# Kernel tuning notes

Measured on AMD Instinct MI355X. Metric: run time of the kernel, lower is better.

The kernel has to match this reference:

```python
import jax, jax.numpy as jnp
import numpy as np

B, T, F_IN = 256, 168, 128
H = 512            # encoder hidden per direction; decoder hidden = 2H
OUT = 1
L_OUT = 48
SCALE = 0.05


def _lstm_scan(x, Wih, Whh, b, h0, c0):
    # x: [T, B, F]; PyTorch LSTM gate order i, f, g, o
    def step(carry, xt):
        h, c = carry
        g = xt @ Wih.T + h @ Whh.T + b
        i, f, gg, o = jnp.split(g, 4, axis=-1)
        c = jax.nn.sigmoid(f) * c + jax.nn.sigmoid(i) * jnp.tanh(gg)
        h = jax.nn.sigmoid(o) * jnp.tanh(c)
        return (h, c), h
    (hT, cT), ys = jax.lax.scan(step, (h0, c0), x)
    return ys, hT, cT


def setup_inputs() -> dict:
    key = jax.random.key(0)
    ks = jax.random.split(key, 16)
    r = lambda k, shp: (jax.random.normal(k, shp, dtype=jnp.float32) * SCALE)
    return {
        "input_seq": jax.random.normal(ks[0], (B, T, F_IN), dtype=jnp.float32),
        "enc_Wih_f": r(ks[1], (4 * H, F_IN)),
        "enc_Whh_f": r(ks[2], (4 * H, H)),
        "enc_bih_f": r(ks[3], (4 * H,)),
        "enc_bhh_f": r(ks[4], (4 * H,)),
        "enc_Wih_b": r(ks[5], (4 * H, F_IN)),
        "enc_Whh_b": r(ks[6], (4 * H, H)),
        "enc_bih_b": r(ks[7], (4 * H,)),
        "enc_bhh_b": r(ks[8], (4 * H,)),
        "dec_Wih": r(ks[9], (4 * 2 * H, OUT)),
        "dec_Whh": r(ks[10], (4 * 2 * H, 2 * H)),
        "dec_bih": r(ks[11], (4 * 2 * H,)),
        "dec_bhh": r(ks[12], (4 * 2 * H,)),
        "fc_W": r(ks[13], (OUT, 2 * H)),
        "fc_b": r(ks[14], (OUT,)),
        "output_length": L_OUT,
    }


def reference(input_seq, enc_Wih_f, enc_Whh_f, enc_bih_f, enc_bhh_f,
              enc_Wih_b, enc_Whh_b, enc_bih_b, enc_bhh_b,
              dec_Wih, dec_Whh, dec_bih, dec_bhh, fc_W, fc_b, output_length):
    b = input_seq.shape[0]
    h = enc_Whh_f.shape[1]
    x = jnp.transpose(input_seq, (1, 0, 2))  # [T, B, F]
    h0 = jnp.zeros((b, h), input_seq.dtype)
    c0 = jnp.zeros((b, h), input_seq.dtype)
    # bidirectional encoder (final hidden/cell only are used downstream)
    _, hf, cf = _lstm_scan(x, enc_Wih_f, enc_Whh_f, enc_bih_f + enc_bhh_f, h0, c0)
    _, hb, cb = _lstm_scan(x[::-1], enc_Wih_b, enc_Whh_b, enc_bih_b + enc_bhh_b, h0, c0)
    # _cat_hidden: concat fwd/bwd states along feature dim -> decoder init state [B, 2H]
    hd = jnp.concatenate([hf, hb], axis=-1)
    cd = jnp.concatenate([cf, cb], axis=-1)
    bd = dec_bih + dec_bhh
    x0 = jnp.zeros((b, fc_W.shape[0]), input_seq.dtype)  # initial decoder input = zeros

    def dec_step(carry, _):
        hh, cc, xt = carry
        g = xt @ dec_Wih.T + hh @ dec_Whh.T + bd
        i, f, gg, o = jnp.split(g, 4, axis=-1)
        cc = jax.nn.sigmoid(f) * cc + jax.nn.sigmoid(i) * jnp.tanh(gg)
        hh = jax.nn.sigmoid(o) * jnp.tanh(cc)
        pred = hh @ fc_W.T + fc_b  # [B, OUT]
        return (hh, cc, pred), pred

    _, preds = jax.lax.scan(dec_step, (hd, cd, x0), None, length=output_length)
    # [L, B, OUT] -> [B, L, OUT] -> squeeze(dim=2) with OUT==1 -> [B, L]
    return jnp.transpose(preds, (1, 0, 2)).squeeze(2)
```

## Files before the change

### kernel.cpp

```cpp
#include <hip/hip_runtime.h>


constexpr int B_ = 256, T_ = 168, F_ = 128, H_ = 512, L_ = 48;
constexpr int KE = F_ + H_;
constexpr int HD = 1024;
constexpr int GE = 4 * H_;
constexpr int EPAD = KE + 8;
constexpr int DPAD = HD + 8;

constexpr int FL256_IDX  = 0;
constexpr int CLAIM_IDX  = 256;
constexpr int ENCF_IDX   = 768;
constexpr int DECF_IDX   = 1280;
constexpr int CLAIM2_IDX = 2048;
constexpr int FL2_IDX    = 2560;

constexpr size_t OFF_SYNC = 0;
constexpr size_t OFF_WCF = 16384;
constexpr size_t OFF_WCB = OFF_WCF + (size_t)GE * KE * 2;
constexpr size_t OFF_PP  = OFF_WCB + (size_t)GE * KE * 2;
constexpr size_t OFF_BF  = OFF_PP  + (size_t)8 * 2 * 64 * 32 * 4;
constexpr size_t OFF_BB  = OFF_BF  + (size_t)GE * 4;
constexpr size_t OFF_XH  = OFF_BB  + (size_t)GE * 4;
constexpr size_t OFF_HE  = OFF_XH  + (size_t)T_ * B_ * F_ * 2;
constexpr size_t OFF_HDD = OFF_HE  + (size_t)2 * 2 * B_ * H_ * 2;
constexpr size_t OFF_CD  = OFF_HDD + (size_t)2 * B_ * HD * 2;

using h8 = __attribute__((ext_vector_type(8))) _Float16;
using f4 = __attribute__((ext_vector_type(4))) float;
using u4 = __attribute__((ext_vector_type(4))) unsigned;

#define DEV static __device__ __forceinline__

DEV float sigm(float x)  { return __fdividef(1.f, 1.f + __expf(-x)); }
DEV float tanh_(float x) { return 1.f - __fdividef(2.f, __expf(2.f * x) + 1.f); }

DEV h8 as_h8(f4 v) { union { f4 f; h8 h; } u; u.f = v; return u.h; }

DEV void astore_u64(void* p, unsigned long long v) {
  __hip_atomic_store((unsigned long long*)p, v, __ATOMIC_RELAXED,
                     __HIP_MEMORY_SCOPE_AGENT);
}
DEV void astore_u32(void* p, unsigned v) {
  __hip_atomic_store((unsigned*)p, v, __ATOMIC_RELAXED, __HIP_MEMORY_SCOPE_AGENT);
}
DEV unsigned aload_u32(const void* p) {
  return __hip_atomic_load((const unsigned*)p, __ATOMIC_RELAXED,
                           __HIP_MEMORY_SCOPE_AGENT);
}
DEV float aload_f32(const void* p) {
  return __hip_atomic_load((const float*)p, __ATOMIC_RELAXED,
                           __HIP_MEMORY_SCOPE_AGENT);
}
DEV void astore_f32(void* p, float v) {
  __hip_atomic_store((float*)p, v, __ATOMIC_RELAXED, __HIP_MEMORY_SCOPE_AGENT);
}
DEV void astore_u16(void* p, _Float16 v) {
  union { _Float16 h; unsigned short s; } u; u.h = v;
  __hip_atomic_store((unsigned short*)p, u.s, __ATOMIC_RELAXED,
                     __HIP_MEMORY_SCOPE_AGENT);
}
DEV void vm_drain() { asm volatile("s_waitcnt vmcnt(0)" ::: "memory"); }

template<bool DEEP>
DEV void ld16(const _Float16* p, f4* A) {
#define L16(FL) asm volatile( \
    "global_load_dwordx4 %0,  %16, off" FL "\n\t" \
    "global_load_dwordx4 %1,  %16, off offset:64" FL "\n\t" \
    "global_load_dwordx4 %2,  %16, off offset:128" FL "\n\t" \
    "global_load_dwordx4 %3,  %16, off offset:192" FL "\n\t" \
    "global_load_dwordx4 %4,  %16, off offset:256" FL "\n\t" \
    "global_load_dwordx4 %5,  %16, off offset:320" FL "\n\t" \
    "global_load_dwordx4 %6,  %16, off offset:384" FL "\n\t" \
    "global_load_dwordx4 %7,  %16, off offset:448" FL "\n\t" \
    "global_load_dwordx4 %8,  %16, off offset:512" FL "\n\t" \
    "global_load_dwordx4 %9,  %16, off offset:576" FL "\n\t" \
    "global_load_dwordx4 %10, %16, off offset:640" FL "\n\t" \
    "global_load_dwordx4 %11, %16, off offset:704" FL "\n\t" \
    "global_load_dwordx4 %12, %16, off offset:768" FL "\n\t" \
    "global_load_dwordx4 %13, %16, off offset:832" FL "\n\t" \
    "global_load_dwordx4 %14, %16, off offset:896" FL "\n\t" \
    "global_load_dwordx4 %15, %16, off offset:960" FL "\n\t" \
    "s_waitcnt vmcnt(0)" \
    : "=&v"(A[0]),"=&v"(A[1]),"=&v"(A[2]),"=&v"(A[3]),"=&v"(A[4]),"=&v"(A[5]), \
      "=&v"(A[6]),"=&v"(A[7]),"=&v"(A[8]),"=&v"(A[9]),"=&v"(A[10]),"=&v"(A[11]), \
      "=&v"(A[12]),"=&v"(A[13]),"=&v"(A[14]),"=&v"(A[15]) \
    : "v"(p) : "memory")
  if constexpr (DEEP) { L16(" sc0 sc1"); } else { L16(" sc0"); }
#undef L16
}

template<bool DEEP>
DEV void ld32(const _Float16* p, f4* A) {
#define L32(FL) asm volatile( \
    "global_load_dwordx4 %0,  %32, off" FL "\n\t" \
    "global_load_dwordx4 %1,  %32, off offset:64" FL "\n\t" \
    "global_load_dwordx4 %2,  %32, off offset:128" FL "\n\t" \
    "global_load_dwordx4 %3,  %32, off offset:192" FL "\n\t" \
    "global_load_dwordx4 %4,  %32, off offset:256" FL "\n\t" \
    "global_load_dwordx4 %5,  %32, off offset:320" FL "\n\t" \
    "global_load_dwordx4 %6,  %32, off offset:384" FL "\n\t" \
    "global_load_dwordx4 %7,  %32, off offset:448" FL "\n\t" \
    "global_load_dwordx4 %8,  %32, off offset:512" FL "\n\t" \
    "global_load_dwordx4 %9,  %32, off offset:576" FL "\n\t" \
    "global_load_dwordx4 %10, %32, off offset:640" FL "\n\t" \
    "global_load_dwordx4 %11, %32, off offset:704" FL "\n\t" \
    "global_load_dwordx4 %12, %32, off offset:768" FL "\n\t" \
    "global_load_dwordx4 %13, %32, off offset:832" FL "\n\t" \
    "global_load_dwordx4 %14, %32, off offset:896" FL "\n\t" \
    "global_load_dwordx4 %15, %32, off offset:960" FL "\n\t" \
    "global_load_dwordx4 %16, %32, off offset:1024" FL "\n\t" \
    "global_load_dwordx4 %17, %32, off offset:1088" FL "\n\t" \
    "global_load_dwordx4 %18, %32, off offset:1152" FL "\n\t" \
    "global_load_dwordx4 %19, %32, off offset:1216" FL "\n\t" \
    "global_load_dwordx4 %20, %32, off offset:1280" FL "\n\t" \
    "global_load_dwordx4 %21, %32, off offset:1344" FL "\n\t" \
    "global_load_dwordx4 %22, %32, off offset:1408" FL "\n\t" \
    "global_load_dwordx4 %23, %32, off offset:1472" FL "\n\t" \
    "global_load_dwordx4 %24, %32, off offset:1536" FL "\n\t" \
    "global_load_dwordx4 %25, %32, off offset:1600" FL "\n\t" \
    "global_load_dwordx4 %26, %32, off offset:1664" FL "\n\t" \
    "global_load_dwordx4 %27, %32, off offset:1728" FL "\n\t" \
    "global_load_dwordx4 %28, %32, off offset:1792" FL "\n\t" \
    "global_load_dwordx4 %29, %32, off offset:1856" FL "\n\t" \
    "global_load_dwordx4 %30, %32, off offset:1920" FL "\n\t" \
    "global_load_dwordx4 %31, %32, off offset:1984" FL "\n\t" \
    "s_waitcnt vmcnt(0)" \
    : "=&v"(A[0]),"=&v"(A[1]),"=&v"(A[2]),"=&v"(A[3]),"=&v"(A[4]),"=&v"(A[5]), \
      "=&v"(A[6]),"=&v"(A[7]),"=&v"(A[8]),"=&v"(A[9]),"=&v"(A[10]),"=&v"(A[11]), \
      "=&v"(A[12]),"=&v"(A[13]),"=&v"(A[14]),"=&v"(A[15]),"=&v"(A[16]),"=&v"(A[17]), \
      "=&v"(A[18]),"=&v"(A[19]),"=&v"(A[20]),"=&v"(A[21]),"=&v"(A[22]),"=&v"(A[23]), \
      "=&v"(A[24]),"=&v"(A[25]),"=&v"(A[26]),"=&v"(A[27]),"=&v"(A[28]),"=&v"(A[29]), \
      "=&v"(A[30]),"=&v"(A[31]) \
    : "v"(p) : "memory")
  if constexpr (DEEP) { L32(" sc0 sc1"); } else { L32(" sc0"); }
#undef L32
}

DEV void ld8x4(const float* p, f4* A) {
  asm volatile(
    "global_load_dwordx4 %0, %8, off sc0 sc1\n\t"
    "global_load_dwordx4 %1, %8, off offset:16 sc0 sc1\n\t"
    "global_load_dwordx4 %2, %8, off offset:32 sc0 sc1\n\t"
    "global_load_dwordx4 %3, %8, off offset:48 sc0 sc1\n\t"
    "global_load_dwordx4 %4, %8, off offset:64 sc0 sc1\n\t"
    "global_load_dwordx4 %5, %8, off offset:80 sc0 sc1\n\t"
    "global_load_dwordx4 %6, %8, off offset:96 sc0 sc1\n\t"
    "global_load_dwordx4 %7, %8, off offset:112 sc0 sc1\n\t"
    "s_waitcnt vmcnt(0)"
    : "=&v"(A[0]),"=&v"(A[1]),"=&v"(A[2]),"=&v"(A[3]),
      "=&v"(A[4]),"=&v"(A[5]),"=&v"(A[6]),"=&v"(A[7])
    : "v"(p) : "memory");
}

DEV unsigned pollflag(const unsigned* p, bool deep) {
  unsigned v;
  if (deep)
    asm volatile("global_load_dword %0, %1, off sc0 sc1\n\t"
                 "s_waitcnt vmcnt(0)" : "=&v"(v) : "v"(p) : "memory");
  else
    asm volatile("global_load_dword %0, %1, off sc0\n\t"
                 "s_waitcnt vmcnt(0)" : "=&v"(v) : "v"(p) : "memory");
  return v;
}
DEV void wait_ge(const unsigned* p, unsigned target, bool deep, int cap) {
  for (int it = 0; it < cap; ++it) {
    unsigned v = pollflag(p, deep);
    if (__ballot(v >= target) == ~0ull) return;
  }
}

DEV void gsync(unsigned* fl, int bi, unsigned phase, int tid) {
  vm_drain();
  __syncthreads();
  if (tid == 0) astore_u32(fl + bi, phase);
  if (tid < 64) {
    const unsigned* p = fl + tid * 4;
    for (int it = 0; it < (1 << 20); ++it) {
      u4 v;
      asm volatile("global_load_dwordx4 %0, %1, off sc0 sc1\n\t"
                   "s_waitcnt vmcnt(0)" : "=&v"(v) : "v"(p) : "memory");
      unsigned a = v[0] < v[1] ? v[0] : v[1];
      unsigned b = v[2] < v[3] ? v[2] : v[3];
      if (__ballot((a < b ? a : b) >= phase) == ~0ull) break;
    }
  }
  __syncthreads();
  asm volatile("" ::: "memory");
}

__global__ void prep_misc(const float* bihF, const float* bhhF,
                          const float* bihB, const float* bhhB, char* ws) {
  int i = blockIdx.x * blockDim.x + threadIdx.x;
  if (i < 2048) astore_u64(ws + (size_t)i * 8, 0ull);
  if (i < GE) {
    ((float*)(ws + OFF_BF))[i] = bihF[i] + bhhF[i];
    ((float*)(ws + OFF_BB))[i] = bihB[i] + bhhB[i];
  }
  if (i < 2 * 2 * B_ * H_ / 4) astore_u64((char*)ws + OFF_HE + (size_t)i * 8, 0ull);
}

__global__ void conv_encw(const float* WihF, const float* WhhF,
                          const float* WihB, const float* WhhB, char* ws) {
  int i = blockIdx.x * blockDim.x + threadIdx.x;
  if (i >= GE * KE) return;
  int r = i / KE, k = i - r * KE;
  float vF = (k < F_) ? WihF[r * F_ + k] : WhhF[r * H_ + (k - F_)];
  float vB = (k < F_) ? WihB[r * F_ + k] : WhhB[r * H_ + (k - F_)];
  ((_Float16*)(ws + OFF_WCF))[i] = (_Float16)vF;
  ((_Float16*)(ws + OFF_WCB))[i] = (_Float16)vB;
}

__global__ void conv_x(const float* x, char* ws) {
  int i = blockIdx.x * blockDim.x + threadIdx.x;
  if (i >= T_ * B_ * F_) return;
  int f = i & 127, b = (i >> 7) & 255, t = i >> 15;
  ((_Float16*)(ws + OFF_XH))[i] = (_Float16)x[((size_t)b * T_ + t) * F_ + f];
}

template<bool LOCAL>
DEV void encoder_phase(int dir, int chunk, int slice,
                       int tid, int wave, int quad, int col, int lane,
                       char* ws, _Float16* lds, _Float16 (*htile)[16]) {
  const _Float16* Wenc  = (const _Float16*)(ws + (dir ? OFF_WCB : OFF_WCF));
  const float*    biasE = (const float*)(ws + (dir ? OFF_BB : OFF_BF));
  const _Float16* Xh    = (const _Float16*)(ws + OFF_XH);
  _Float16* hE = (_Float16*)(ws + OFF_HE);
  _Float16* hD = (_Float16*)(ws + OFF_HDD);
  float*    cD = (float*)(ws + OFF_CD);
  unsigned* encf = (unsigned*)ws + ENCF_IDX + (dir * 4 + chunk) * 64;

  const int j0 = slice * 16;
  const int mb = chunk * 64;

  for (int it = 0; it < 20; ++it) {
    int idx = it * 256 + tid;
    int n = idx / 80, e = idx - n * 80;
    int g = n >> 4, u = n & 15;
    *((h8*)(lds + n * EPAD) + e) =
        *((const h8*)(Wenc + (size_t)(g * H_ + j0 + u) * KE) + e);
  }
  float breg[4];
#pragma unroll
  for (int g = 0; g < 4; ++g) breg[g] = biasE[g * H_ + j0 + col];
  float cst[4] = {0.f, 0.f, 0.f, 0.f};
  __syncthreads();

  h8 Bf[4][16];
#pragma unroll
  for (int g = 0; g < 4; ++g)
#pragma unroll
    for (int kk = 0; kk < 16; ++kk)
      Bf[g][kk] = *((const h8*)(lds + (g * 16 + col) * EPAD + F_) + kk * 4 + quad);

  const int arow = mb + wave * 16 + col;
  const int mrow = mb + wave * 16 + quad * 4;

  for (int t = 0; t < T_; ++t) {
    const int par = t & 1;
    const int tx  = dir ? (T_ - 1 - t) : t;
    f4 z = {0.f, 0.f, 0.f, 0.f};
    f4 acc[4] = {z, z, z, z};

    const h8* xr = (const h8*)(Xh + ((size_t)tx * B_ + arow) * F_);
#pragma unroll
    for (int kk = 0; kk < 4; ++kk) {
      h8 a = xr[kk * 4 + quad];
#pragma unroll
      for (int g = 0; g < 4; ++g) {
        h8 b = *((const h8*)(lds + (g * 16 + col) * EPAD) + kk * 4 + quad);
        acc[g] = __builtin_amdgcn_mfma_f32_16x16x32_f16(a, b, acc[g], 0, 0, 0);
      }
    }
    if (t > 0)
      wait_ge(encf + (lane & 31), (unsigned)t, !LOCAL, 1 << 16);
    f4 A[16];
    ld16<!LOCAL>(hE + ((size_t)(par * 2 + dir) * B_ + arow) * H_ + quad * 8, A);
#pragma unroll
    for (int kk = 0; kk < 16; ++kk) {
      h8 a = as_h8(A[kk]);
#pragma unroll
      for (int g = 0; g < 4; ++g)
        acc[g] = __builtin_amdgcn_mfma_f32_16x16x32_f16(a, Bf[g][kk], acc[g], 0, 0, 0);
    }

#pragma unroll
    for (int r = 0; r < 4; ++r) {
      float gi = acc[0][r] + breg[0];
      float gf = acc[1][r] + breg[1];
      float gg = acc[2][r] + breg[2];
      float go = acc[3][r] + breg[3];
      float c = sigm(gf) * cst[r] + sigm(gi) * tanh_(gg);
      cst[r] = c;
      float h = sigm(go) * tanh_(c);
      htile[wave * 16 + quad * 4 + r][col] = (_Float16)h;
      if (t == T_ - 1)
        astore_f32(&cD[(size_t)(mrow + r) * HD + dir * H_ + j0 + col], c);
    }
    __syncthreads();
    if (tid < 128) {
      int row = tid >> 1, half = tid & 1;
      const unsigned long long* src =
          (const unsigned long long*)&htile[row][half * 8];
      if (t < T_ - 1) {
        _Float16* dst = hE + ((size_t)((par ^ 1) * 2 + dir) * B_ + mb + row) * H_ +
                        j0 + half * 8;
        if (LOCAL) {
          ((unsigned long long*)dst)[0] = src[0];
          ((unsigned long long*)(dst + 4))[0] = src[1];
        } else {
          astore_u64(dst, src[0]);
          astore_u64(dst + 4, src[1]);
        }
      } else {
        _Float16* dst = hD + (size_t)(mb + row) * HD + dir * H_ + j0 + half * 8;
        astore_u64(dst, src[0]);
        astore_u64(dst + 4, src[1]);
      }
    }
    vm_drain();
    __syncthreads();
    if (tid == 0 && t < T_ - 1) {
      if (LOCAL) *(volatile unsigned*)(encf + slice) = (unsigned)(t + 1);
      else       astore_u32(encf + slice, (unsigned)(t + 1));
    }
  }
}

DEV void decoder_phase(int xcd, int rank, int tid, int wave, int quad, int col,
                       int lane, const float* dWih, const float* dWhh,
                       const float* dbih, const float* dbhh, const float* fcW,
                       const float* fcb, float* out, char* ws, _Float16* lds,
                       float* predbuf, float (*ppsum)[32]) {
  _Float16* hdd = (_Float16*)(ws + OFF_HDD);
  float* cD = (float*)(ws + OFF_CD);
  float* PP = (float*)(ws + OFF_PP) + (size_t)xcd * 2 * 32 * 32;
  unsigned* decf = (unsigned*)ws + DECF_IDX + xcd * 64;

  const int j0b = rank * 32;
  const int R0  = xcd * 32;
  const int m   = wave & 1;
  const int uh  = wave >> 1;
  const int unit = j0b + uh * 16 + col;
  const int arow = R0 + m * 16 + col;
  const int mrow = R0 + m * 16 + quad * 4;

  for (int it = 0; it < 64; ++it) {
    int idx = it * 256 + tid;
    int n = idx >> 8, c = idx & 255;
    int srow = (n >> 5) * HD + j0b + (n & 31);
    f4 w = *((const f4*)(dWhh + (size_t)srow * HD + c * 4));
    union { _Float16 h[4]; unsigned long long q; } u2;
#pragma unroll
    for (int i2 = 0; i2 < 4; ++i2) u2.h[i2] = (_Float16)w[i2];
    *(unsigned long long*)(lds + n * DPAD + c * 4) = u2.q;
  }
  h8 Bf[2][32];
#pragma unroll
  for (int gg = 0; gg < 2; ++gg)
#pragma unroll
    for (int kk = 0; kk < 32; ++kk) {
      const float* src = dWhh + (size_t)((2 + gg) * HD + unit) * HD + kk * 32 + quad * 8;
      f4 w0 = *((const f4*)src);
      f4 w1 = *((const f4*)(src + 4));
      union { _Float16 h[8]; h8 v; } u3;
#pragma unroll
      for (int i2 = 0; i2 < 4; ++i2) {
        u3.h[i2]     = (_Float16)w0[i2];
        u3.h[4 + i2] = (_Float16)w1[i2];
      }
      Bf[gg][kk] = u3.v;
    }
  float breg[4], wreg[4];
#pragma unroll
  for (int g = 0; g < 4; ++g) {
    breg[g] = dbih[g * HD + unit] + dbhh[g * HD + unit];
    wreg[g] = dWih[g * HD + unit];
  }
  const float fcw = fcW[unit];
  const float fb  = fcb[0];
  float cst[4];
#pragma unroll
  for (int r = 0; r < 4; ++r)
    cst[r] = aload_f32(cD + (size_t)(mrow + r) * HD + unit);
  __syncthreads();

  for (int l = 0; l <= L_; ++l) {
    float predv = 0.f;
    if (l > 0) {
      wait_ge(decf + (lane & 31), (unsigned)l, true, 1 << 16);
      const float* PPr = PP + (size_t)((l - 1) & 1) * 32 * 32;
      int row = lane & 31;
      f4 pv[8];
      ld8x4(PPr + (size_t)row * 32, pv);
      float s = 0.f;
#pragma unroll
      for (int j = 0; j < 8; ++j) {
        s += pv[j][0]; s += pv[j][1]; s += pv[j][2]; s += pv[j][3];
      }
      predv = s + fb;
      if (rank == 0 && wave == 0 && lane < 32)
        predbuf[(l - 1) * 32 + lane] = predv;
    }
    if (l == L_) break;
    const int par = l & 1;

    f4 A[32];
    ld32<true>(hdd + ((size_t)par * B_ + arow) * HD + quad * 8, A);

    f4 z = {0.f, 0.f, 0.f, 0.f};
    f4 acc[4] = {z, z, z, z};
#pragma unroll
    for (int kk = 0; kk < 32; ++kk) {
      h8 a = as_h8(A[kk]);
      h8 b0 = *((const h8*)(lds + (0 * 32 + uh * 16 + col) * DPAD) + kk * 4 + quad);
      h8 b1 = *((const h8*)(lds + (1 * 32 + uh * 16 + col) * DPAD) + kk * 4 + quad);
      acc[0] = __builtin_amdgcn_mfma_f32_16x16x32_f16(a, b0, acc[0], 0, 0, 0);
      acc[1] = __builtin_amdgcn_mfma_f32_16x16x32_f16(a, b1, acc[1], 0, 0, 0);
      acc[2] = __builtin_amdgcn_mfma_f32_16x16x32_f16(a, Bf[0][kk], acc[2], 0, 0, 0);
      acc[3] = __builtin_amdgcn_mfma_f32_16x16x32_f16(a, Bf[1][kk], acc[3], 0, 0, 0);
    }

    float pr[4], sum[4];
#pragma unroll
    for (int r = 0; r < 4; ++r)
      pr[r] = (l > 0) ? __shfl(predv, m * 16 + quad * 4 + r) : 0.f;
#pragma unroll
    for (int r = 0; r < 4; ++r) {
      float gi = acc[0][r] + breg[0] + pr[r] * wreg[0];
      float gf = acc[1][r] + breg[1] + pr[r] * wreg[1];
      float gg = acc[2][r] + breg[2] + pr[r] * wreg[2];
      float go = acc[3][r] + breg[3] + pr[r] * wreg[3];
      float c = sigm(gf) * cst[r] + sigm(gi) * tanh_(gg);
      cst[r] = c;
      float h = sigm(go) * tanh_(c);
      size_t hoff = ((size_t)(par ^ 1) * B_ + mrow + r) * HD + unit;
      astore_u16(hdd + hoff, (_Float16)h);
      sum[r] = h * fcw;
    }
#pragma unroll
    for (int off = 1; off < 16; off <<= 1) {
#pragma unroll
      for (int r = 0; r < 4; ++r) sum[r] += __shfl_xor(sum[r], off, 16);
    }
    if (col == 0) {
#pragma unroll
      for (int r = 0; r < 4; ++r)
        ppsum[uh][m * 16 + quad * 4 + r] = sum[r];
    }
    __syncthreads();
    if (tid < 32) {
      float v = ppsum[0][tid] + ppsum[1][tid];
      float* PPw = PP + (size_t)(l & 1) * 32 * 32;
      astore_f32(PPw + (size_t)tid * 32 + rank, v);
    }
    vm_drain();
    __syncthreads();
    if (tid == 0) astore_u32(decf + rank, (unsigned)(l + 1));
  }

  if (rank == 0) {
    __syncthreads();
    for (int idx = tid; idx < L_ * 32; idx += 256) {
      int row2 = idx & 31, st = idx >> 5;
      out[(size_t)(R0 + row2) * L_ + st] = predbuf[st * 32 + row2];
    }
  }
}

__global__ __launch_bounds__(256, 1)
void enc_kernel(char* __restrict__ ws) {
  __shared__ __align__(16) _Float16 lds[64 * EPAD];
  __shared__ __align__(16) _Float16 htile[64][16];
  __shared__ int sh[2];

  const int tid  = threadIdx.x;
  const int wave = tid >> 6;
  const int lane = tid & 63;
  const int quad = lane >> 4;
  const int col  = lane & 15;
  const int bi   = blockIdx.x;

  unsigned* sync  = (unsigned*)(ws + OFF_SYNC);
  unsigned* fl    = sync + FL256_IDX;
  unsigned* claim = sync + CLAIM_IDX;

  if (tid == 0) {
    unsigned x;
    asm volatile("s_getreg_b32 %0, hwreg(HW_REG_XCC_ID)" : "=s"(x));
    int xcd = (int)(x & 7u);
    unsigned r = __hip_atomic_fetch_add(claim + xcd * 64, 1u, __ATOMIC_RELAXED,
                                        __HIP_MEMORY_SCOPE_AGENT);
    sh[0] = xcd;
    sh[1] = (int)r;
  }
  __syncthreads();
  const int xcd = sh[0], rank = sh[1];
  gsync(fl, bi, 1u, tid);
  if (tid == 0) {
    int d = 0;
    for (int k = 0; k < 8; ++k)
      if (aload_u32(claim + k * 64) != 32u) d = 1;
    sh[0] = d;
  }
  __syncthreads();
  const bool deg = (sh[0] != 0) || (rank >= 32);

  if (!deg)
    encoder_phase<true>(xcd >> 2, xcd & 3, rank, tid, wave, quad, col, lane,
                        ws, lds, htile);
  else
    encoder_phase<false>(bi >> 7, bi & 3, (bi & 127) >> 2, tid, wave, quad, col,
                         lane, ws, lds, htile);
}

__global__ __launch_bounds__(256, 1)
void dec_kernel(const float* __restrict__ dWih, const float* __restrict__ dWhh,
                const float* __restrict__ dbih, const float* __restrict__ dbhh,
                const float* __restrict__ fcW, const float* __restrict__ fcb,
                float* __restrict__ out, char* __restrict__ ws) {
  __shared__ __align__(16) _Float16 lds[64 * DPAD];
  __shared__ __align__(16) float predbuf[L_ * 32];
  __shared__ __align__(16) float ppsum[2][32];
  __shared__ int sh[2];

  const int tid  = threadIdx.x;
  const int wave = tid >> 6;
  const int lane = tid & 63;
  const int quad = lane >> 4;
  const int col  = lane & 15;
  const int bi   = blockIdx.x;

  unsigned* sync  = (unsigned*)(ws + OFF_SYNC);
  unsigned* fl2   = sync + FL2_IDX;
  unsigned* claim = sync + CLAIM2_IDX;

  if (tid == 0) {
    unsigned x;
    asm volatile("s_getreg_b32 %0, hwreg(HW_REG_XCC_ID)" : "=s"(x));
    int xcd = (int)(x & 7u);
    unsigned r = __hip_atomic_fetch_add(claim + xcd * 64, 1u, __ATOMIC_RELAXED,
                                        __HIP_MEMORY_SCOPE_AGENT);
    sh[0] = xcd;
    sh[1] = (int)r;
  }
  __syncthreads();
  const int xcd = sh[0], rank = sh[1];
  gsync(fl2, bi, 1u, tid);
  if (tid == 0) {
    int d = 0;
    for (int k = 0; k < 8; ++k)
      if (aload_u32(claim + k * 64) != 32u) d = 1;
    sh[0] = d;
  }
  __syncthreads();
  const bool deg = (sh[0] != 0) || (rank >= 32);

  if (!deg)
    decoder_phase(xcd, rank, tid, wave, quad, col, lane, dWih, dWhh,
                  dbih, dbhh, fcW, fcb, out, ws, lds, predbuf, ppsum);
  else
    decoder_phase(bi >> 5, bi & 31, tid, wave, quad, col, lane, dWih,
                  dWhh, dbih, dbhh, fcW, fcb, out, ws, lds, predbuf, ppsum);
}

extern "C" void kernel_launch(void* const* d_in, const int* in_sizes, int n_in,
                              void* d_out, int out_size, void* d_ws, size_t ws_size,
                              hipStream_t stream) {
  const float* x     = (const float*)d_in[0];
  const float* eWihF = (const float*)d_in[1];
  const float* eWhhF = (const float*)d_in[2];
  const float* ebihF = (const float*)d_in[3];
  const float* ebhhF = (const float*)d_in[4];
  const float* eWihB = (const float*)d_in[5];
  const float* eWhhB = (const float*)d_in[6];
  const float* ebihB = (const float*)d_in[7];
  const float* ebhhB = (const float*)d_in[8];
  const float* dWih  = (const float*)d_in[9];
  const float* dWhh  = (const float*)d_in[10];
  const float* dbih  = (const float*)d_in[11];
  const float* dbhh  = (const float*)d_in[12];
  const float* fcW   = (const float*)d_in[13];
  const float* fcb   = (const float*)d_in[14];
  float* out = (float*)d_out;
  char*  ws  = (char*)d_ws;

  prep_misc<<<512, 256, 0, stream>>>(ebihF, ebhhF, ebihB, ebhhB, ws);
  conv_encw<<<(GE * KE) / 256, 256, 0, stream>>>(eWihF, eWhhF, eWihB, eWhhB, ws);
  conv_x<<<(T_ * B_ * F_) / 256, 256, 0, stream>>>(x, ws);

  enc_kernel<<<dim3(256), dim3(256), 0, stream>>>(ws);
  dec_kernel<<<dim3(256), dim3(256), 0, stream>>>(dWih, dWhh, dbih, dbhh,
                                                  fcW, fcb, out, ws);
}
```

Baseline: 1.544 ms.

## Compute decoder prediction via MFMA on full hidden state instead of cross-block partial sums

Each decoder block now recomputes the fc projection (prediction) redundantly from the full fp16 hidden state it already loads, using an MFMA against fc weights held in LDS with only one output column non-zero. This removes the per-step partial-sum reduction: the shuffle reduction, the LDS exchange, an extra __syncthreads, the global partial-product writes and the dependent global reads after the flag wait. In exchange every block does 32 extra MFMAs per step. The prediction is now computed from the fp16-rounded hidden state with fp16 fc weights, which lowers precision.

```diff
diff --git a/kernel.cpp b/kernel.cpp
--- a/kernel.cpp
+++ b/kernel.cpp
@@ -137,22 +137,6 @@
 #undef L32
 }
 
-DEV void ld8x4(const float* p, f4* A) {
-  asm volatile(
-    "global_load_dwordx4 %0, %8, off sc0 sc1\n\t"
-    "global_load_dwordx4 %1, %8, off offset:16 sc0 sc1\n\t"
-    "global_load_dwordx4 %2, %8, off offset:32 sc0 sc1\n\t"
-    "global_load_dwordx4 %3, %8, off offset:48 sc0 sc1\n\t"
-    "global_load_dwordx4 %4, %8, off offset:64 sc0 sc1\n\t"
-    "global_load_dwordx4 %5, %8, off offset:80 sc0 sc1\n\t"
-    "global_load_dwordx4 %6, %8, off offset:96 sc0 sc1\n\t"
-    "global_load_dwordx4 %7, %8, off offset:112 sc0 sc1\n\t"
-    "s_waitcnt vmcnt(0)"
-    : "=&v"(A[0]),"=&v"(A[1]),"=&v"(A[2]),"=&v"(A[3]),
-      "=&v"(A[4]),"=&v"(A[5]),"=&v"(A[6]),"=&v"(A[7])
-    : "v"(p) : "memory");
-}
-
 DEV unsigned pollflag(const unsigned* p, bool deep) {
   unsigned v;
   if (deep)
@@ -331,10 +315,9 @@
                        int lane, const float* dWih, const float* dWhh,
                        const float* dbih, const float* dbhh, const float* fcW,
                        const float* fcb, float* out, char* ws, _Float16* lds,
-                       float* predbuf, float (*ppsum)[32]) {
+                       float* predbuf, _Float16* fcwlds) {
   _Float16* hdd = (_Float16*)(ws + OFF_HDD);
   float* cD = (float*)(ws + OFF_CD);
-  float* PP = (float*)(ws + OFF_PP) + (size_t)xcd * 2 * 32 * 32;
   unsigned* decf = (unsigned*)ws + DECF_IDX + xcd * 64;
 
   const int j0b = rank * 32;
@@ -345,6 +328,8 @@
   const int arow = R0 + m * 16 + col;
   const int mrow = R0 + m * 16 + quad * 4;
 
+  for (int i = tid; i < HD; i += 256) fcwlds[i] = (_Float16)fcW[i];
+
   for (int it = 0; it < 64; ++it) {
     int idx = it * 256 + tid;
     int n = idx >> 8, c = idx & 255;
@@ -377,38 +362,40 @@
     breg[g] = dbih[g * HD + unit] + dbhh[g * HD + unit];
     wreg[g] = dWih[g * HD + unit];
   }
-  const float fcw = fcW[unit];
-  const float fb  = fcb[0];
+  const float fb = fcb[0];
   float cst[4];
 #pragma unroll
   for (int r = 0; r < 4; ++r)
     cst[r] = aload_f32(cD + (size_t)(mrow + r) * HD + unit);
   __syncthreads();
 
+  const f4 z = {0.f, 0.f, 0.f, 0.f};
+  const h8 hz = as_h8(z);
+
   for (int l = 0; l <= L_; ++l) {
-    float predv = 0.f;
-    if (l > 0) {
+    if (l > 0)
       wait_ge(decf + (lane & 31), (unsigned)l, true, 1 << 16);
-      const float* PPr = PP + (size_t)((l - 1) & 1) * 32 * 32;
-      int row = lane & 31;
-      f4 pv[8];
-      ld8x4(PPr + (size_t)row * 32, pv);
-      float s = 0.f;
-#pragma unroll
-      for (int j = 0; j < 8; ++j) {
-        s += pv[j][0]; s += pv[j][1]; s += pv[j][2]; s += pv[j][3];
-      }
-      predv = s + fb;
-      if (rank == 0 && wave == 0 && lane < 32)
-        predbuf[(l - 1) * 32 + lane] = predv;
-    }
-    if (l == L_) break;
     const int par = l & 1;
 
     f4 A[32];
     ld32<true>(hdd + ((size_t)par * B_ + arow) * HD + quad * 8, A);
 
-    f4 z = {0.f, 0.f, 0.f, 0.f};
+    f4 accp = z;
+    if (l > 0) {
+#pragma unroll
+      for (int kk = 0; kk < 32; ++kk) {
+        h8 bw = *((const h8*)(fcwlds + kk * 32 + quad * 8));
+        bw = (col == 0) ? bw : hz;
+        accp = __builtin_amdgcn_mfma_f32_16x16x32_f16(as_h8(A[kk]), bw, accp, 0, 0, 0);
+      }
+      if (rank == 0 && uh == 0 && col == 0) {
+#pragma unroll
+        for (int r = 0; r < 4; ++r)
+          predbuf[(l - 1) * 32 + m * 16 + quad * 4 + r] = accp[r] + fb;
+      }
+    }
+    if (l == L_) break;
+
     f4 acc[4] = {z, z, z, z};
 #pragma unroll
     for (int kk = 0; kk < 32; ++kk) {
@@ -421,10 +408,11 @@
       acc[3] = __builtin_amdgcn_mfma_f32_16x16x32_f16(a, Bf[1][kk], acc[3], 0, 0, 0);
     }
 
-    float pr[4], sum[4];
+    float pr[4];
 #pragma unroll
     for (int r = 0; r < 4; ++r)
-      pr[r] = (l > 0) ? __shfl(predv, m * 16 + quad * 4 + r) : 0.f;
+      pr[r] = (l > 0) ? (__shfl(accp[r], quad * 16) + fb) : 0.f;
+
 #pragma unroll
     for (int r = 0; r < 4; ++r) {
       float gi = acc[0][r] + breg[0] + pr[r] * wreg[0];
@@ -436,23 +424,6 @@
       float h = sigm(go) * tanh_(c);
       size_t hoff = ((size_t)(par ^ 1) * B_ + mrow + r) * HD + unit;
       astore_u16(hdd + hoff, (_Float16)h);
-      sum[r] = h * fcw;
-    }
-#pragma unroll
-    for (int off = 1; off < 16; off <<= 1) {
-#pragma unroll
-      for (int r = 0; r < 4; ++r) sum[r] += __shfl_xor(sum[r], off, 16);
-    }
-    if (col == 0) {
-#pragma unroll
-      for (int r = 0; r < 4; ++r)
-        ppsum[uh][m * 16 + quad * 4 + r] = sum[r];
-    }
-    __syncthreads();
-    if (tid < 32) {
-      float v = ppsum[0][tid] + ppsum[1][tid];
-      float* PPw = PP + (size_t)(l & 1) * 32 * 32;
-      astore_f32(PPw + (size_t)tid * 32 + rank, v);
     }
     vm_drain();
     __syncthreads();
@@ -521,7 +492,7 @@
                 float* __restrict__ out, char* __restrict__ ws) {
   __shared__ __align__(16) _Float16 lds[64 * DPAD];
   __shared__ __align__(16) float predbuf[L_ * 32];
-  __shared__ __align__(16) float ppsum[2][32];
+  __shared__ __align__(16) _Float16 fcwlds[HD];
   __shared__ int sh[2];
 
   const int tid  = threadIdx.x;
@@ -558,10 +529,10 @@
 
   if (!deg)
     decoder_phase(xcd, rank, tid, wave, quad, col, lane, dWih, dWhh,
-                  dbih, dbhh, fcW, fcb, out, ws, lds, predbuf, ppsum);
+                  dbih, dbhh, fcW, fcb, out, ws, lds, predbuf, fcwlds);
   else
     decoder_phase(bi >> 5, bi & 31, tid, wave, quad, col, lane, dWih,
-                  dWhh, dbih, dbhh, fcW, fcb, out, ws, lds, predbuf, ppsum);
+                  dWhh, dbih, dbhh, fcW, fcb, out, ws, lds, predbuf, fcwlds);
 }
 
 extern "C" void kernel_launch(void* const* d_in, const int* in_sizes, int n_in,
```

Measured after the change: 1.574 ms. No clear change (+2.0%).
